# Optimization experiments

Measured on AMD Instinct MI355X. Metric: run time of the kernel, lower is better.

The kernel has to match this reference:

```python
import jax, jax.numpy as jnp
import numpy as np

B, S, D, H, A = 2, 2048, 1024, 16, 64
INIT_STD = 0.02


def setup_inputs() -> dict:
    key = jax.random.key(0)
    ks = jax.random.split(key, 5)
    return {
        "residual": jax.random.normal(ks[0], (B, S, D), dtype=jnp.float32),
        "Wq": jax.random.normal(ks[1], (H, D, A), dtype=jnp.float32) * INIT_STD,
        "Wk": jax.random.normal(ks[2], (H, D, A), dtype=jnp.float32) * INIT_STD,
        "Wv": jax.random.normal(ks[3], (H, D, A), dtype=jnp.float32) * INIT_STD,
        "Wo": jax.random.normal(ks[4], (H, A, D), dtype=jnp.float32) * INIT_STD,
        "bq": jnp.zeros((H, A), dtype=jnp.float32),
        "bk": jnp.zeros((H, A), dtype=jnp.float32),
        "bv": jnp.zeros((H, A), dtype=jnp.float32),
        "bo": jnp.zeros((D,), dtype=jnp.float32),
    }


def reference(residual, Wq, Wk, Wv, Wo, bq, bk, bv, bo):
    # residual: [B,S,D]; W{q,k,v}: [H,D,A]; Wo: [H,A,D]
    q = jnp.einsum("bsd,hda->bhsa", residual, Wq) + bq[None, :, None, :]
    k = jnp.einsum("bsd,hda->bhsa", residual, Wk) + bk[None, :, None, :]
    v = jnp.einsum("bsd,hda->bhsa", residual, Wv) + bv[None, :, None, :]
    scale = 1.0 / jnp.sqrt(jnp.float32(q.shape[-1]))
    scores = jnp.einsum("bhsa,bhta->bhst", q, k) * scale  # [B,H,S,S]
    s = scores.shape[-1]
    causal = jnp.tril(jnp.ones((s, s), dtype=bool))  # True = keep
    # original masked_fill with -100000.0 (not -inf); stay faithful
    masked = jnp.where(causal, scores, jnp.float32(-100000.0))
    pattern = jax.nn.softmax(masked, axis=-1)
    z = jnp.einsum("bhst,bhta->bshа".replace("а", "a"), pattern, v)  # [B,S,H,A]
    out = jnp.einsum("bsha,had->bsd", z, Wo) + bo
    return out
```

## Files before the change

### kernel.cpp

```cpp
#include <hip/hip_runtime.h>
#include <hip/hip_bf16.h>

#define B_ 2
#define S_ 2048
#define D_ 1024
#define H_ 16
#define A_ 64

typedef __attribute__((ext_vector_type(8))) short bf16x8;
typedef __attribute__((ext_vector_type(4))) float f32x4;
typedef __attribute__((ext_vector_type(4))) unsigned int u32x4;
typedef __attribute__((ext_vector_type(2))) unsigned int u32x2;

#define QSCALE 0.1803368801111204f

__device__ inline short f2bf(float f) {
    union { float f; unsigned u; } x; x.f = f;
    unsigned r = x.u + 0x7fff + ((x.u >> 16) & 1);
    return (short)(r >> 16);
}

__device__ inline unsigned cvt_pk_bf16(float lo, float hi) {
    unsigned r;
    asm("v_cvt_pk_bf16_f32 %0, %1, %2" : "=v"(r) : "v"(lo), "v"(hi));
    return r;
}
__device__ inline void pl32swap(unsigned &a, unsigned &b) {
    u32x2 r = __builtin_amdgcn_permlane32_swap(a, b, false, false);
    a = r[0]; b = r[1];
}
__device__ inline void pl16swap(unsigned &a, unsigned &b) {
    u32x2 r = __builtin_amdgcn_permlane16_swap(a, b, false, false);
    a = r[0]; b = r[1];
}
__device__ inline float cross_quad_max(float x) {
    unsigned a = __builtin_bit_cast(unsigned, x), b = a;
    pl32swap(a, b);
    float y = fmaxf(__builtin_bit_cast(float, a), __builtin_bit_cast(float, b));
    unsigned c = __builtin_bit_cast(unsigned, y), d = c;
    pl16swap(c, d);
    return fmaxf(__builtin_bit_cast(float, c), __builtin_bit_cast(float, d));
}
__device__ inline float cross_quad_sum(float x) {
    unsigned a = __builtin_bit_cast(unsigned, x), b = a;
    pl32swap(a, b);
    float y = __builtin_bit_cast(float, a) + __builtin_bit_cast(float, b);
    unsigned c = __builtin_bit_cast(unsigned, y), d = c;
    pl16swap(c, d);
    return __builtin_bit_cast(float, c) + __builtin_bit_cast(float, d);
}

__global__ __launch_bounds__(256) void cast_kernel(const float* __restrict__ x,
                                                   short* __restrict__ y, int n) {
    int i = (blockIdx.x * 256 + threadIdx.x) * 8;
    if (i < n) {
        float4 a = *(const float4*)(x + i);
        float4 b = *(const float4*)(x + i + 4);
        bf16x8 o;
        o[0]=f2bf(a.x); o[1]=f2bf(a.y); o[2]=f2bf(a.z); o[3]=f2bf(a.w);
        o[4]=f2bf(b.x); o[5]=f2bf(b.y); o[6]=f2bf(b.z); o[7]=f2bf(b.w);
        *(bf16x8*)(y + i) = o;
    }
}

__global__ __launch_bounds__(256) void wtrans_kernel(
    const float* __restrict__ Wq, const float* __restrict__ Wk,
    const float* __restrict__ Wv, const float* __restrict__ Wo,
    short* __restrict__ Wt, short* __restrict__ Wot) {
    const int kt = blockIdx.x, yy = blockIdx.y, z = blockIdx.z;
    __shared__ short T[64 * 72];
    const int tid = threadIdx.x;
    const int r = tid >> 2, c0 = (tid & 3) * 16;
    const float* src;
    if (z < 3) {
        const float* W = z == 0 ? Wq : (z == 1 ? Wk : Wv);
        src = &W[yy * (D_ * A_) + (kt * 64 + r) * A_ + c0];
    } else {
        src = &Wo[(kt * 64 + r) * D_ + yy * 64 + c0];
    }
    #pragma unroll
    for (int q = 0; q < 4; q++) {
        float4 f = *(const float4*)(src + q * 4);
        T[r * 72 + c0 + q * 4 + 0] = f2bf(f.x);
        T[r * 72 + c0 + q * 4 + 1] = f2bf(f.y);
        T[r * 72 + c0 + q * 4 + 2] = f2bf(f.z);
        T[r * 72 + c0 + q * 4 + 3] = f2bf(f.w);
    }
    __syncthreads();
    const int a = tid >> 2, kc = (tid & 3) * 16;
    bf16x8 o0, o1;
    #pragma unroll
    for (int j = 0; j < 8; j++) {
        o0[j] = T[(kc + j) * 72 + a];
        o1[j] = T[(kc + 8 + j) * 72 + a];
    }
    const int n_base = (z < 3) ? z * 1024 + yy * 64 : yy * 64;
    short* dst = (z < 3) ? &Wt[(n_base + a) * D_ + kt * 64 + kc]
                         : &Wot[(n_base + a) * D_ + kt * 64 + kc];
    *(bf16x8*)dst = o0;
    *(bf16x8*)(dst + 8) = o1;
}

__global__ __launch_bounds__(256) void qkv_gemm(
    const short* __restrict__ X, const short* __restrict__ Wt,
    const float* __restrict__ bq, const float* __restrict__ bk, const float* __restrict__ bv,
    short* __restrict__ Qb, short* __restrict__ Kb, short* __restrict__ Vt) {
    const int mt = blockIdx.x, nt = blockIdx.y;
    const int m0 = mt * 128, n0 = nt * 128;
    const int sel = n0 >> 10;
    __shared__ short Xl[2][128 * 40], Wl[2][128 * 40];
    const int tid = threadIdx.x, wv = tid >> 6, lane = tid & 63, quad = lane >> 4, l16 = lane & 15;
    const int grow = tid >> 1, gk = (tid & 1) * 16;
    f32x4 acc[4][4] = {};
    bf16x8 xr0, xr1, wr0, wr1;
    {
        const short* xs = &X[(m0 + grow) * D_ + gk];
        xr0 = *(const bf16x8*)xs; xr1 = *(const bf16x8*)(xs + 8);
        const short* wsp = &Wt[(n0 + grow) * D_ + gk];
        wr0 = *(const bf16x8*)wsp; wr1 = *(const bf16x8*)(wsp + 8);
    }
    const int rm = (wv & 1) * 64, cn = (wv >> 1) * 64;
    for (int i = 0; i < 32; i++) {
        const int bu = i & 1;
        *(bf16x8*)&Xl[bu][grow * 40 + gk]     = xr0;
        *(bf16x8*)&Xl[bu][grow * 40 + gk + 8] = xr1;
        *(bf16x8*)&Wl[bu][grow * 40 + gk]     = wr0;
        *(bf16x8*)&Wl[bu][grow * 40 + gk + 8] = wr1;
        __syncthreads();
        if (i < 31) {
            const int k0 = (i + 1) * 32;
            const short* xs = &X[(m0 + grow) * D_ + k0 + gk];
            xr0 = *(const bf16x8*)xs; xr1 = *(const bf16x8*)(xs + 8);
            const short* wsp = &Wt[(n0 + grow) * D_ + k0 + gk];
            wr0 = *(const bf16x8*)wsp; wr1 = *(const bf16x8*)(wsp + 8);
        }
        bf16x8 af[4];
        #pragma unroll
        for (int rt = 0; rt < 4; rt++)
            af[rt] = *(bf16x8*)&Xl[bu][(rm + rt * 16 + l16) * 40 + quad * 8];
        #pragma unroll
        for (int ct = 0; ct < 4; ct++) {
            bf16x8 bf = *(bf16x8*)&Wl[bu][(cn + ct * 16 + l16) * 40 + quad * 8];
            #pragma unroll
            for (int rt = 0; rt < 4; rt++)
                acc[rt][ct] = __builtin_amdgcn_mfma_f32_16x16x32_bf16(af[rt], bf, acc[rt][ct], 0, 0, 0);
        }
    }
    const int b = m0 >> 11;
    const float* bias = sel == 0 ? bq : (sel == 1 ? bk : bv);
    if (sel < 2) {
        short* dst = sel == 0 ? Qb : Kb;
        const float scale = sel == 0 ? QSCALE : 1.0f;
        #pragma unroll
        for (int ct = 0; ct < 4; ct++) {
            const int n = n0 + cn + ct * 16 + l16;
            const int h = (n >> 6) & 15, a = n & 63;
            const float bi = bias[n & 1023];
            #pragma unroll
            for (int rt = 0; rt < 4; rt++)
                #pragma unroll
                for (int r = 0; r < 4; r++) {
                    const int row = m0 + rm + rt * 16 + quad * 4 + r;
                    const int s = row & (S_ - 1);
                    dst[(((b * H_) + h) * S_ + s) * A_ + a] = f2bf((acc[rt][ct][r] + bi) * scale);
                }
        }
    } else {
        #pragma unroll
        for (int ct = 0; ct < 4; ct++) {
            const int n = n0 + cn + ct * 16 + l16;
            const int h = (n >> 6) & 15, a = n & 63;
            const float bi = bias[n & 1023];
            #pragma unroll
            for (int rt = 0; rt < 4; rt++) {
                short4 pk;
                pk.x = f2bf(acc[rt][ct][0] + bi);
                pk.y = f2bf(acc[rt][ct][1] + bi);
                pk.z = f2bf(acc[rt][ct][2] + bi);
                pk.w = f2bf(acc[rt][ct][3] + bi);
                const int row = m0 + rm + rt * 16 + quad * 4;
                const int s = row & (S_ - 1);
                *(short4*)&Vt[(((b * H_) + h) * A_ + a) * S_ + s] = pk;
            }
        }
    }
}

__global__ __launch_bounds__(512, 4) void flash_kernel(
    const short* __restrict__ Qb, const short* __restrict__ Kb,
    const short* __restrict__ Vt, short* __restrict__ Z) {
    const int p = blockIdx.x, h = blockIdx.y, b = blockIdx.z;
    const int bh = b * H_ + h;
    const int qlo = p, qhi = 31 - p;
    __shared__ short Kl[2][4096], Vl[2][4096];
    const int tid = threadIdx.x, wv = tid >> 6, lane = tid & 63, quad = lane >> 4, l16 = lane & 15;
    const int wg = wv & 3;
    const int myqt = (wv < 4) ? qhi : qlo;
    const int qpos = wg * 16 + l16;

    const int L = tid;
    const int srow = (L >> 7) * 16 + (L & 15);
    const int scol = ((L >> 6) & 1) * 32 + ((L >> 4) & 3) * 8;

    const short* qptr = &Qb[(bh * S_ + myqt * 64 + wg * 16 + l16) * A_ + quad * 8];
    bf16x8 qf[2] = { *(const bf16x8*)qptr, *(const bf16x8*)(qptr + 32) };

    f32x4 O[4] = {};
    float m_i = -1e30f, l_i = 0.f;

    bf16x8 kreg = *(const bf16x8*)&Kb[(bh * S_ + srow) * A_ + scol];
    bf16x8 vreg = *(const bf16x8*)&Vt[(bh * A_ + srow) * S_ + scol];

    for (int kt = 0; kt <= qhi; kt++) {
        const int bu = kt & 1;
        *(bf16x8*)&Kl[bu][L * 8] = kreg;
        *(bf16x8*)&Vl[bu][L * 8] = vreg;
        __syncthreads();
        if (kt < qhi) {
            kreg = *(const bf16x8*)&Kb[(bh * S_ + (kt + 1) * 64 + srow) * A_ + scol];
            vreg = *(const bf16x8*)&Vt[(bh * A_ + srow) * S_ + (kt + 1) * 64 + scol];
        }
        if (kt <= myqt) {
            f32x4 sacc[4] = {};
            #pragma unroll
            for (int kk = 0; kk < 2; kk++)
                #pragma unroll
                for (int ct = 0; ct < 4; ct++) {
                    bf16x8 kf = *(bf16x8*)&Kl[bu][((ct * 2 + kk) * 64 + lane) * 8];
                    sacc[ct] = __builtin_amdgcn_mfma_f32_16x16x32_bf16(kf, qf[kk], sacc[ct], 0, 0, 0);
                }
            if (kt == myqt) {
                #pragma unroll
                for (int ct = 0; ct < 4; ct++)
                    #pragma unroll
                    for (int r = 0; r < 4; r++)
                        if (ct * 16 + quad * 4 + r > qpos) sacc[ct][r] = -1e30f;
            }
            f32x4 t4;
            #pragma unroll
            for (int r = 0; r < 4; r++)
                t4[r] = fmaxf(fmaxf(sacc[0][r], sacc[1][r]), fmaxf(sacc[2][r], sacc[3][r]));
            float vmax = fmaxf(fmaxf(t4[0], t4[1]), fmaxf(t4[2], t4[3]));
            vmax = cross_quad_max(vmax);
            const float mn = fmaxf(m_i, vmax);
            const float alpha = exp2f(m_i - mn);
            m_i = mn;
            #pragma unroll
            for (int ct = 0; ct < 4; ct++)
                #pragma unroll
                for (int r = 0; r < 4; r++)
                    sacc[ct][r] = exp2f(sacc[ct][r] - mn);
            f32x4 ps;
            #pragma unroll
            for (int r = 0; r < 4; r++)
                ps[r] = (sacc[0][r] + sacc[1][r]) + (sacc[2][r] + sacc[3][r]);
            float rs = (ps[0] + ps[1]) + (ps[2] + ps[3]);
            rs = cross_quad_sum(rs);
            l_i = l_i * alpha + rs;
            #pragma unroll
            for (int ct = 0; ct < 4; ct++) O[ct] *= alpha;
            #pragma unroll
            for (int kk = 0; kk < 2; kk++) {
                unsigned A0 = cvt_pk_bf16(sacc[2 * kk][0], sacc[2 * kk][1]);
                unsigned A1 = cvt_pk_bf16(sacc[2 * kk][2], sacc[2 * kk][3]);
                unsigned B0 = cvt_pk_bf16(sacc[2 * kk + 1][0], sacc[2 * kk + 1][1]);
                unsigned B1 = cvt_pk_bf16(sacc[2 * kk + 1][2], sacc[2 * kk + 1][3]);
                pl32swap(A0, B0);
                pl16swap(A0, B0);
                pl32swap(A1, B1);
                pl16swap(A1, B1);
                u32x4 wu; wu[0] = A0; wu[1] = A1; wu[2] = B0; wu[3] = B1;
                bf16x8 pb = __builtin_bit_cast(bf16x8, wu);
                #pragma unroll
                for (int ct = 0; ct < 4; ct++) {
                    bf16x8 vf = *(bf16x8*)&Vl[bu][((ct * 2 + kk) * 64 + lane) * 8];
                    O[ct] = __builtin_amdgcn_mfma_f32_16x16x32_bf16(vf, pb, O[ct], 0, 0, 0);
                }
            }
        }
    }
    const float inv = 1.0f / l_i;
    const int s = myqt * 64 + wg * 16 + l16;
    #pragma unroll
    for (int ct = 0; ct < 4; ct++) {
        short4 o4;
        o4.x = f2bf(O[ct][0] * inv);
        o4.y = f2bf(O[ct][1] * inv);
        o4.z = f2bf(O[ct][2] * inv);
        o4.w = f2bf(O[ct][3] * inv);
        *(short4*)&Z[(b * S_ + s) * (H_ * A_) + h * A_ + ct * 16 + quad * 4] = o4;
    }
}

__global__ __launch_bounds__(256) void proj_gemm(
    const short* __restrict__ Zb, const short* __restrict__ Wot,
    const float* __restrict__ bo, float* __restrict__ out) {
    const int mt = blockIdx.x, nt = blockIdx.y;
    const int m0 = mt * 128, n0 = nt * 64;
    __shared__ short Xl[2][128 * 40], Wl[2][64 * 40];
    const int tid = threadIdx.x, wv = tid >> 6, lane = tid & 63, quad = lane >> 4, l16 = lane & 15;
    const int grow = tid >> 1, gk = (tid & 1) * 16;
    const bool doW = (tid < 128);
    f32x4 acc[4][2] = {};
    bf16x8 xr0, xr1, wr0, wr1;
    {
        const short* xs = &Zb[(m0 + grow) * D_ + gk];
        xr0 = *(const bf16x8*)xs; xr1 = *(const bf16x8*)(xs + 8);
        if (doW) {
            const short* wsp = &Wot[(n0 + grow) * D_ + gk];
            wr0 = *(const bf16x8*)wsp; wr1 = *(const bf16x8*)(wsp + 8);
        }
    }
    const int rm = (wv & 1) * 64, cn = (wv >> 1) * 32;
    for (int i = 0; i < 32; i++) {
        const int bu = i & 1;
        *(bf16x8*)&Xl[bu][grow * 40 + gk]     = xr0;
        *(bf16x8*)&Xl[bu][grow * 40 + gk + 8] = xr1;
        if (doW) {
            *(bf16x8*)&Wl[bu][grow * 40 + gk]     = wr0;
            *(bf16x8*)&Wl[bu][grow * 40 + gk + 8] = wr1;
        }
        __syncthreads();
        if (i < 31) {
            const int k0 = (i + 1) * 32;
            const short* xs = &Zb[(m0 + grow) * D_ + k0 + gk];
            xr0 = *(const bf16x8*)xs; xr1 = *(const bf16x8*)(xs + 8);
            if (doW) {
                const short* wsp = &Wot[(n0 + grow) * D_ + k0 + gk];
                wr0 = *(const bf16x8*)wsp; wr1 = *(const bf16x8*)(wsp + 8);
            }
        }
        bf16x8 af[4];
        #pragma unroll
        for (int rt = 0; rt < 4; rt++)
            af[rt] = *(bf16x8*)&Xl[bu][(rm + rt * 16 + l16) * 40 + quad * 8];
        #pragma unroll
        for (int ct = 0; ct < 2; ct++) {
            bf16x8 bf = *(bf16x8*)&Wl[bu][(cn + ct * 16 + l16) * 40 + quad * 8];
            #pragma unroll
            for (int rt = 0; rt < 4; rt++)
                acc[rt][ct] = __builtin_amdgcn_mfma_f32_16x16x32_bf16(af[rt], bf, acc[rt][ct], 0, 0, 0);
        }
    }
    #pragma unroll
    for (int ct = 0; ct < 2; ct++) {
        const int n = n0 + cn + ct * 16 + l16;
        const float bi = bo[n];
        #pragma unroll
        for (int rt = 0; rt < 4; rt++)
            #pragma unroll
            for (int r = 0; r < 4; r++) {
                const int row = m0 + rm + rt * 16 + quad * 4 + r;
                out[row * D_ + n] = acc[rt][ct][r] + bi;
            }
    }
}

extern "C" void kernel_launch(void* const* d_in, const int* in_sizes, int n_in,
                              void* d_out, int out_size, void* d_ws, size_t ws_size,
                              hipStream_t stream) {
    const float* residual = (const float*)d_in[0];
    const float* Wq = (const float*)d_in[1];
    const float* Wk = (const float*)d_in[2];
    const float* Wv = (const float*)d_in[3];
    const float* Wo = (const float*)d_in[4];
    const float* bq = (const float*)d_in[5];
    const float* bk = (const float*)d_in[6];
    const float* bv = (const float*)d_in[7];
    const float* bo = (const float*)d_in[8];
    float* out = (float*)d_out;

    char* ws = (char*)d_ws;
    const size_t NE = (size_t)B_ * S_ * D_;
    short* Xbf = (short*)(ws);
    short* Wt  = (short*)(ws +  8ull * 1024 * 1024);
    short* Wot = (short*)(ws + 14ull * 1024 * 1024);
    short* Qb  = (short*)(ws + 16ull * 1024 * 1024);
    short* Kb  = (short*)(ws + 24ull * 1024 * 1024);
    short* Vt  = (short*)(ws + 32ull * 1024 * 1024);
    short* Zb  = (short*)(ws + 40ull * 1024 * 1024);

    hipLaunchKernelGGL(cast_kernel, dim3((int)(NE / (256 * 8))), dim3(256), 0, stream,
                       residual, Xbf, (int)NE);
    hipLaunchKernelGGL(wtrans_kernel, dim3(16, 16, 4), dim3(256), 0, stream,
                       Wq, Wk, Wv, Wo, Wt, Wot);
    hipLaunchKernelGGL(qkv_gemm, dim3(32, 24), dim3(256), 0, stream,
                       Xbf, Wt, bq, bk, bv, Qb, Kb, Vt);
    hipLaunchKernelGGL(flash_kernel, dim3(16, H_, B_), dim3(512), 0, stream,
                       Qb, Kb, Vt, Zb);
    hipLaunchKernelGGL(proj_gemm, dim3(32, 16), dim3(256), 0, stream,
                       Zb, Wot, bo, out);
}
```

Baseline: 199.1 us.

## Replace paired causal q-tile blocks with one q-tile per 256-thread block

The flash attention kernel previously paired query tiles p and 31-p in one 512-thread block to balance causal work, with both halves sharing each K/V tile load. Now each 256-thread block handles a single 64-row query tile over a grid of 32×H×B, and each thread loads two K/V chunks. This makes blocks smaller and more numerous and removes the idle-wave branch. It gives up the shared K/V loads across the pair, so total K/V traffic roughly doubles, and it brings back an imbalanced causal workload across blocks.

```diff
diff --git a/kernel.cpp b/kernel.cpp
--- a/kernel.cpp
+++ b/kernel.cpp
@@ -186,101 +186,105 @@
     }
 }
 
-__global__ __launch_bounds__(512, 4) void flash_kernel(
+__global__ __launch_bounds__(256, 4) void flash_kernel(
     const short* __restrict__ Qb, const short* __restrict__ Kb,
     const short* __restrict__ Vt, short* __restrict__ Z) {
-    const int p = blockIdx.x, h = blockIdx.y, b = blockIdx.z;
+    const int qt = blockIdx.x, h = blockIdx.y, b = blockIdx.z;
     const int bh = b * H_ + h;
-    const int qlo = p, qhi = 31 - p;
     __shared__ short Kl[2][4096], Vl[2][4096];
     const int tid = threadIdx.x, wv = tid >> 6, lane = tid & 63, quad = lane >> 4, l16 = lane & 15;
-    const int wg = wv & 3;
-    const int myqt = (wv < 4) ? qhi : qlo;
-    const int qpos = wg * 16 + l16;
-
-    const int L = tid;
-    const int srow = (L >> 7) * 16 + (L & 15);
-    const int scol = ((L >> 6) & 1) * 32 + ((L >> 4) & 3) * 8;
-
-    const short* qptr = &Qb[(bh * S_ + myqt * 64 + wg * 16 + l16) * A_ + quad * 8];
+    const int qpos = wv * 16 + l16;
+
+    const int L0 = tid, L1 = tid + 256;
+    const int srow0 = (L0 >> 7) * 16 + (L0 & 15);
+    const int scol0 = ((L0 >> 6) & 1) * 32 + ((L0 >> 4) & 3) * 8;
+    const int srow1 = (L1 >> 7) * 16 + (L1 & 15);
+    const int scol1 = ((L1 >> 6) & 1) * 32 + ((L1 >> 4) & 3) * 8;
+
+    const short* qptr = &Qb[(bh * S_ + qt * 64 + qpos) * A_ + quad * 8];
     bf16x8 qf[2] = { *(const bf16x8*)qptr, *(const bf16x8*)(qptr + 32) };
 
     f32x4 O[4] = {};
     float m_i = -1e30f, l_i = 0.f;
 
-    bf16x8 kreg = *(const bf16x8*)&Kb[(bh * S_ + srow) * A_ + scol];
-    bf16x8 vreg = *(const bf16x8*)&Vt[(bh * A_ + srow) * S_ + scol];
-
-    for (int kt = 0; kt <= qhi; kt++) {
+    bf16x8 kreg0 = *(const bf16x8*)&Kb[(bh * S_ + srow0) * A_ + scol0];
+    bf16x8 kreg1 = *(const bf16x8*)&Kb[(bh * S_ + srow1) * A_ + scol1];
+    bf16x8 vreg0 = *(const bf16x8*)&Vt[(bh * A_ + srow0) * S_ + scol0];
+    bf16x8 vreg1 = *(const bf16x8*)&Vt[(bh * A_ + srow1) * S_ + scol1];
+
+    for (int kt = 0; kt <= qt; kt++) {
         const int bu = kt & 1;
-        *(bf16x8*)&Kl[bu][L * 8] = kreg;
-        *(bf16x8*)&Vl[bu][L * 8] = vreg;
+        *(bf16x8*)&Kl[bu][L0 * 8] = kreg0;
+        *(bf16x8*)&Kl[bu][L1 * 8] = kreg1;
+        *(bf16x8*)&Vl[bu][L0 * 8] = vreg0;
+        *(bf16x8*)&Vl[bu][L1 * 8] = vreg1;
         __syncthreads();
-        if (kt < qhi) {
-            kreg = *(const bf16x8*)&Kb[(bh * S_ + (kt + 1) * 64 + srow) * A_ + scol];
-            vreg = *(const bf16x8*)&Vt[(bh * A_ + srow) * S_ + (kt + 1) * 64 + scol];
-        }
-        if (kt <= myqt) {
-            f32x4 sacc[4] = {};
-            #pragma unroll
-            for (int kk = 0; kk < 2; kk++)
-                #pragma unroll
-                for (int ct = 0; ct < 4; ct++) {
-                    bf16x8 kf = *(bf16x8*)&Kl[bu][((ct * 2 + kk) * 64 + lane) * 8];
-                    sacc[ct] = __builtin_amdgcn_mfma_f32_16x16x32_bf16(kf, qf[kk], sacc[ct], 0, 0, 0);
-                }
-            if (kt == myqt) {
-                #pragma unroll
-                for (int ct = 0; ct < 4; ct++)
-                    #pragma unroll
-                    for (int r = 0; r < 4; r++)
-                        if (ct * 16 + quad * 4 + r > qpos) sacc[ct][r] = -1e30f;
-            }
-            f32x4 t4;
-            #pragma unroll
-            for (int r = 0; r < 4; r++)
-                t4[r] = fmaxf(fmaxf(sacc[0][r], sacc[1][r]), fmaxf(sacc[2][r], sacc[3][r]));
-            float vmax = fmaxf(fmaxf(t4[0], t4[1]), fmaxf(t4[2], t4[3]));
-            vmax = cross_quad_max(vmax);
-            const float mn = fmaxf(m_i, vmax);
-            const float alpha = exp2f(m_i - mn);
-            m_i = mn;
+        if (kt < qt) {
+            const int s1 = (kt + 1) * 64;
+            kreg0 = *(const bf16x8*)&Kb[(bh * S_ + s1 + srow0) * A_ + scol0];
+            kreg1 = *(const bf16x8*)&Kb[(bh * S_ + s1 + srow1) * A_ + scol1];
+            vreg0 = *(const bf16x8*)&Vt[(bh * A_ + srow0) * S_ + s1 + scol0];
+            vreg1 = *(const bf16x8*)&Vt[(bh * A_ + srow1) * S_ + s1 + scol1];
+        }
+        f32x4 sacc[4] = {};
+        #pragma unroll
+        for (int kk = 0; kk < 2; kk++)
+            #pragma unroll
+            for (int ct = 0; ct < 4; ct++) {
+                bf16x8 kf = *(bf16x8*)&Kl[bu][((ct * 2 + kk) * 64 + lane) * 8];
+                sacc[ct] = __builtin_amdgcn_mfma_f32_16x16x32_bf16(kf, qf[kk], sacc[ct], 0, 0, 0);
+            }
+        if (kt == qt) {
             #pragma unroll
             for (int ct = 0; ct < 4; ct++)
                 #pragma unroll
                 for (int r = 0; r < 4; r++)
-                    sacc[ct][r] = exp2f(sacc[ct][r] - mn);
-            f32x4 ps;
+                    if (ct * 16 + quad * 4 + r > qpos) sacc[ct][r] = -1e30f;
+        }
+        f32x4 t4;
+        #pragma unroll
+        for (int r = 0; r < 4; r++)
+            t4[r] = fmaxf(fmaxf(sacc[0][r], sacc[1][r]), fmaxf(sacc[2][r], sacc[3][r]));
+        float vmax = fmaxf(fmaxf(t4[0], t4[1]), fmaxf(t4[2], t4[3]));
+        vmax = cross_quad_max(vmax);
+        const float mn = fmaxf(m_i, vmax);
+        const float alpha = exp2f(m_i - mn);
+        m_i = mn;
+        #pragma unroll
+        for (int ct = 0; ct < 4; ct++)
             #pragma unroll
             for (int r = 0; r < 4; r++)
-                ps[r] = (sacc[0][r] + sacc[1][r]) + (sacc[2][r] + sacc[3][r]);
-            float rs = (ps[0] + ps[1]) + (ps[2] + ps[3]);
-            rs = cross_quad_sum(rs);
-            l_i = l_i * alpha + rs;
-            #pragma unroll
-            for (int ct = 0; ct < 4; ct++) O[ct] *= alpha;
-            #pragma unroll
-            for (int kk = 0; kk < 2; kk++) {
-                unsigned A0 = cvt_pk_bf16(sacc[2 * kk][0], sacc[2 * kk][1]);
-                unsigned A1 = cvt_pk_bf16(sacc[2 * kk][2], sacc[2 * kk][3]);
-                unsigned B0 = cvt_pk_bf16(sacc[2 * kk + 1][0], sacc[2 * kk + 1][1]);
-                unsigned B1 = cvt_pk_bf16(sacc[2 * kk + 1][2], sacc[2 * kk + 1][3]);
-                pl32swap(A0, B0);
-                pl16swap(A0, B0);
-                pl32swap(A1, B1);
-                pl16swap(A1, B1);
-                u32x4 wu; wu[0] = A0; wu[1] = A1; wu[2] = B0; wu[3] = B1;
-                bf16x8 pb = __builtin_bit_cast(bf16x8, wu);
-                #pragma unroll
-                for (int ct = 0; ct < 4; ct++) {
-                    bf16x8 vf = *(bf16x8*)&Vl[bu][((ct * 2 + kk) * 64 + lane) * 8];
-                    O[ct] = __builtin_amdgcn_mfma_f32_16x16x32_bf16(vf, pb, O[ct], 0, 0, 0);
-                }
+                sacc[ct][r] = exp2f(sacc[ct][r] - mn);
+        f32x4 ps;
+        #pragma unroll
+        for (int r = 0; r < 4; r++)
+            ps[r] = (sacc[0][r] + sacc[1][r]) + (sacc[2][r] + sacc[3][r]);
+        float rs = (ps[0] + ps[1]) + (ps[2] + ps[3]);
+        rs = cross_quad_sum(rs);
+        l_i = l_i * alpha + rs;
+        #pragma unroll
+        for (int ct = 0; ct < 4; ct++) O[ct] *= alpha;
+        #pragma unroll
+        for (int kk = 0; kk < 2; kk++) {
+            unsigned A0 = cvt_pk_bf16(sacc[2 * kk][0], sacc[2 * kk][1]);
+            unsigned A1 = cvt_pk_bf16(sacc[2 * kk][2], sacc[2 * kk][3]);
+            unsigned B0 = cvt_pk_bf16(sacc[2 * kk + 1][0], sacc[2 * kk + 1][1]);
+            unsigned B1 = cvt_pk_bf16(sacc[2 * kk + 1][2], sacc[2 * kk + 1][3]);
+            pl32swap(A0, B0);
+            pl16swap(A0, B0);
+            pl32swap(A1, B1);
+            pl16swap(A1, B1);
+            u32x4 wu; wu[0] = A0; wu[1] = A1; wu[2] = B0; wu[3] = B1;
+            bf16x8 pb = __builtin_bit_cast(bf16x8, wu);
+            #pragma unroll
+            for (int ct = 0; ct < 4; ct++) {
+                bf16x8 vf = *(bf16x8*)&Vl[bu][((ct * 2 + kk) * 64 + lane) * 8];
+                O[ct] = __builtin_amdgcn_mfma_f32_16x16x32_bf16(vf, pb, O[ct], 0, 0, 0);
             }
         }
     }
     const float inv = 1.0f / l_i;
-    const int s = myqt * 64 + wg * 16 + l16;
+    const int s = qt * 64 + qpos;
     #pragma unroll
     for (int ct = 0; ct < 4; ct++) {
         short4 o4;
@@ -386,7 +390,7 @@
                        Wq, Wk, Wv, Wo, Wt, Wot);
     hipLaunchKernelGGL(qkv_gemm, dim3(32, 24), dim3(256), 0, stream,
                        Xbf, Wt, bq, bk, bv, Qb, Kb, Vt);
-    hipLaunchKernelGGL(flash_kernel, dim3(16, H_, B_), dim3(512), 0, stream,
+    hipLaunchKernelGGL(flash_kernel, dim3(32, H_, B_), dim3(256), 0, stream,
                        Qb, Kb, Vt, Zb);
     hipLaunchKernelGGL(proj_gemm, dim3(32, 16), dim3(256), 0, stream,
                        Zb, Wot, bo, out);
```

New measurement: 226.6 us. +13.8%, slower.

## Stage GEMM tiles via direct global-to-LDS loads in QKV and proj GEMMs

Applied to the files above, without the earlier changes.

Replaces the register-staged global loads plus LDS stores in the QKV and output-projection GEMMs with global_load_lds direct-to-LDS transfers. The next K tile is prefetched into the other buffer, with a barrier at the end of each iteration. The intent is to cut VGPR pressure and the separate LDS store instructions. In exchange the padded row stride (40) becomes an unpadded stride of 32, which can raise LDS bank conflicts on the fragment reads. The code also relies on the implicit waitcnt at the barrier to make the async loads visible.

```diff
diff --git a/kernel.cpp b/kernel.cpp
--- a/kernel.cpp
+++ b/kernel.cpp
@@ -18,6 +18,12 @@
     union { float f; unsigned u; } x; x.f = f;
     unsigned r = x.u + 0x7fff + ((x.u >> 16) & 1);
     return (short)(r >> 16);
+}
+
+__device__ __forceinline__ void gld16(const short* g, short* l) {
+    __builtin_amdgcn_global_load_lds(
+        (const __attribute__((address_space(1))) unsigned int*)g,
+        (__attribute__((address_space(3))) unsigned int*)l, 16, 0, 0);
 }
 
 __device__ inline unsigned cvt_pk_bf16(float lo, float hi) {
@@ -108,44 +114,42 @@
     const int mt = blockIdx.x, nt = blockIdx.y;
     const int m0 = mt * 128, n0 = nt * 128;
     const int sel = n0 >> 10;
-    __shared__ short Xl[2][128 * 40], Wl[2][128 * 40];
+    __shared__ short Xl[2][4096], Wl[2][4096];
     const int tid = threadIdx.x, wv = tid >> 6, lane = tid & 63, quad = lane >> 4, l16 = lane & 15;
-    const int grow = tid >> 1, gk = (tid & 1) * 16;
+    const int srow = tid >> 2, schunk = (tid & 3) * 8;
     f32x4 acc[4][4] = {};
-    bf16x8 xr0, xr1, wr0, wr1;
-    {
-        const short* xs = &X[(m0 + grow) * D_ + gk];
-        xr0 = *(const bf16x8*)xs; xr1 = *(const bf16x8*)(xs + 8);
-        const short* wsp = &Wt[(n0 + grow) * D_ + gk];
-        wr0 = *(const bf16x8*)wsp; wr1 = *(const bf16x8*)(wsp + 8);
-    }
+    const short* pA0 = &X [(m0      + srow) * D_ + schunk];
+    const short* pA1 = &X [(m0 + 64 + srow) * D_ + schunk];
+    const short* pB0 = &Wt[(n0      + srow) * D_ + schunk];
+    const short* pB1 = &Wt[(n0 + 64 + srow) * D_ + schunk];
+
+    #define QSTAGE(bu, off) do { \
+        gld16(pA0 + (off), &Xl[bu][tid * 8]); \
+        gld16(pA1 + (off), &Xl[bu][2048 + tid * 8]); \
+        gld16(pB0 + (off), &Wl[bu][tid * 8]); \
+        gld16(pB1 + (off), &Wl[bu][2048 + tid * 8]); \
+    } while (0)
+
+    QSTAGE(0, 0);
+    __syncthreads();
     const int rm = (wv & 1) * 64, cn = (wv >> 1) * 64;
     for (int i = 0; i < 32; i++) {
         const int bu = i & 1;
-        *(bf16x8*)&Xl[bu][grow * 40 + gk]     = xr0;
-        *(bf16x8*)&Xl[bu][grow * 40 + gk + 8] = xr1;
-        *(bf16x8*)&Wl[bu][grow * 40 + gk]     = wr0;
-        *(bf16x8*)&Wl[bu][grow * 40 + gk + 8] = wr1;
-        __syncthreads();
-        if (i < 31) {
-            const int k0 = (i + 1) * 32;
-            const short* xs = &X[(m0 + grow) * D_ + k0 + gk];
-            xr0 = *(const bf16x8*)xs; xr1 = *(const bf16x8*)(xs + 8);
-            const short* wsp = &Wt[(n0 + grow) * D_ + k0 + gk];
-            wr0 = *(const bf16x8*)wsp; wr1 = *(const bf16x8*)(wsp + 8);
-        }
+        if (i < 31) QSTAGE(bu ^ 1, (i + 1) * 32);
         bf16x8 af[4];
         #pragma unroll
         for (int rt = 0; rt < 4; rt++)
-            af[rt] = *(bf16x8*)&Xl[bu][(rm + rt * 16 + l16) * 40 + quad * 8];
+            af[rt] = *(bf16x8*)&Xl[bu][(rm + rt * 16 + l16) * 32 + quad * 8];
         #pragma unroll
         for (int ct = 0; ct < 4; ct++) {
-            bf16x8 bf = *(bf16x8*)&Wl[bu][(cn + ct * 16 + l16) * 40 + quad * 8];
+            bf16x8 bf = *(bf16x8*)&Wl[bu][(cn + ct * 16 + l16) * 32 + quad * 8];
             #pragma unroll
             for (int rt = 0; rt < 4; rt++)
                 acc[rt][ct] = __builtin_amdgcn_mfma_f32_16x16x32_bf16(af[rt], bf, acc[rt][ct], 0, 0, 0);
         }
-    }
+        __syncthreads();
+    }
+    #undef QSTAGE
     const int b = m0 >> 11;
     const float* bias = sel == 0 ? bq : (sel == 1 ? bk : bv);
     if (sel < 2) {
@@ -297,51 +301,40 @@
     const float* __restrict__ bo, float* __restrict__ out) {
     const int mt = blockIdx.x, nt = blockIdx.y;
     const int m0 = mt * 128, n0 = nt * 64;
-    __shared__ short Xl[2][128 * 40], Wl[2][64 * 40];
+    __shared__ short Xl[2][4096], Wl[2][2048];
     const int tid = threadIdx.x, wv = tid >> 6, lane = tid & 63, quad = lane >> 4, l16 = lane & 15;
-    const int grow = tid >> 1, gk = (tid & 1) * 16;
-    const bool doW = (tid < 128);
+    const int srow = tid >> 2, schunk = (tid & 3) * 8;
     f32x4 acc[4][2] = {};
-    bf16x8 xr0, xr1, wr0, wr1;
-    {
-        const short* xs = &Zb[(m0 + grow) * D_ + gk];
-        xr0 = *(const bf16x8*)xs; xr1 = *(const bf16x8*)(xs + 8);
-        if (doW) {
-            const short* wsp = &Wot[(n0 + grow) * D_ + gk];
-            wr0 = *(const bf16x8*)wsp; wr1 = *(const bf16x8*)(wsp + 8);
-        }
-    }
+    const short* pA0 = &Zb [(m0      + srow) * D_ + schunk];
+    const short* pA1 = &Zb [(m0 + 64 + srow) * D_ + schunk];
+    const short* pB0 = &Wot[(n0      + srow) * D_ + schunk];
+
+    #define PSTAGE(bu, off) do { \
+        gld16(pA0 + (off), &Xl[bu][tid * 8]); \
+        gld16(pA1 + (off), &Xl[bu][2048 + tid * 8]); \
+        gld16(pB0 + (off), &Wl[bu][tid * 8]); \
+    } while (0)
+
+    PSTAGE(0, 0);
+    __syncthreads();
     const int rm = (wv & 1) * 64, cn = (wv >> 1) * 32;
     for (int i = 0; i < 32; i++) {
         const int bu = i & 1;
-        *(bf16x8*)&Xl[bu][grow * 40 + gk]     = xr0;
-        *(bf16x8*)&Xl[bu][grow * 40 + gk + 8] = xr1;
-        if (doW) {
-            *(bf16x8*)&Wl[bu][grow * 40 + gk]     = wr0;
-            *(bf16x8*)&Wl[bu][grow * 40 + gk + 8] = wr1;
-        }
-        __syncthreads();
-        if (i < 31) {
-            const int k0 = (i + 1) * 32;
-            const short* xs = &Zb[(m0 + grow) * D_ + k0 + gk];
-            xr0 = *(const bf16x8*)xs; xr1 = *(const bf16x8*)(xs + 8);
-            if (doW) {
-                const short* wsp = &Wot[(n0 + grow) * D_ + k0 + gk];
-                wr0 = *(const bf16x8*)wsp; wr1 = *(const bf16x8*)(wsp + 8);
-            }
-        }
+        if (i < 31) PSTAGE(bu ^ 1, (i + 1) * 32);
         bf16x8 af[4];
         #pragma unroll
         for (int rt = 0; rt < 4; rt++)
-            af[rt] = *(bf16x8*)&Xl[bu][(rm + rt * 16 + l16) * 40 + quad * 8];
+            af[rt] = *(bf16x8*)&Xl[bu][(rm + rt * 16 + l16) * 32 + quad * 8];
         #pragma unroll
         for (int ct = 0; ct < 2; ct++) {
-            bf16x8 bf = *(bf16x8*)&Wl[bu][(cn + ct * 16 + l16) * 40 + quad * 8];
+            bf16x8 bf = *(bf16x8*)&Wl[bu][(cn + ct * 16 + l16) * 32 + quad * 8];
             #pragma unroll
             for (int rt = 0; rt < 4; rt++)
                 acc[rt][ct] = __builtin_amdgcn_mfma_f32_16x16x32_bf16(af[rt], bf, acc[rt][ct], 0, 0, 0);
         }
-    }
+        __syncthreads();
+    }
+    #undef PSTAGE
     #pragma unroll
     for (int ct = 0; ct < 2; ct++) {
         const int n = n0 + cn + ct * 16 + l16;
```

Measured after the change: 204.1 us. 1.03x slower.
